# Performance work log

Measured on AMD Instinct MI355X. Metric: run time of the kernel, lower is better.

The kernel has to match this reference:

```python
import jax, jax.numpy as jnp
import numpy as np

NHEADS = 16
SCALE_BASE = 512
GN_EPS = 1e-5


def rotate_every_two(x):
    x1 = x[..., ::2]
    x2 = x[..., 1::2]
    return jnp.stack((-x2, x1), axis=-1).reshape(x.shape)


def xpos_apply(x, downscale, offset=0):
    # x: [B, T, C]; XPOS over the FULL embedding dim (applied before head split)
    B, T, C = x.shape
    half = C // 2
    scale_vec = (jnp.arange(0, C, 2, dtype=jnp.float32) + 0.4 * C) / (1.4 * C)  # [half]
    min_pos = -(T + offset) // 2
    max_pos = T + offset + min_pos
    power = jnp.arange(min_pos, max_pos, dtype=jnp.float32) / SCALE_BASE  # [L]
    scale = scale_vec[None, :] ** power[:, None]  # [L, half]
    L = scale.shape[0]
    inv_freq = 1.0 / (10000.0 ** (jnp.arange(half, dtype=jnp.float32) / half))
    sinusoid = jnp.arange(L, dtype=jnp.float32)[:, None] * inv_freq[None, :]  # [L, half]
    sin, cos = jnp.sin(sinusoid), jnp.cos(sinusoid)
    if L > T:
        scale, sin, cos = scale[-T:], sin[-T:], cos[-T:]
    if downscale:
        scale = 1.0 / scale
    sin = jnp.repeat(sin * scale, 2, axis=-1)  # [T, C] (duplicate_interleave)
    cos = jnp.repeat(cos * scale, 2, axis=-1)
    return x * cos + rotate_every_two(x) * sin


def decay_mask(nheads, T):
    gamma = 1.0 - 2.0 ** (-5.0 - jnp.arange(nheads, dtype=jnp.float32))  # [H]
    idx = jnp.arange(T)
    diff = idx[:, None] - idx[None, :]  # [T, T]
    keep = diff >= 0
    m = gamma[:, None, None] ** jnp.where(keep, diff, 0).astype(jnp.float32)
    return jnp.where(keep[None, :, :], m, 0.0)  # [H, T, T]


def setup_inputs() -> dict:
    key = jax.random.key(0)
    ks = jax.random.split(key, 6)
    B, T, C = 2, 2048, 1024
    w_std = 0.02
    return {
        "x": jax.random.normal(ks[0], (B, T, C), jnp.float32),
        "w_qkvff": jax.random.normal(ks[1], (5 * C, C), jnp.float32) * w_std,
        "w_gated": jax.random.normal(ks[2], (C, C), jnp.float32) * w_std,
        "b_gated": jnp.zeros((C,), jnp.float32),
        "w_proj": jax.random.normal(ks[3], (C, C), jnp.float32) * w_std,
        "b_proj": jnp.zeros((C,), jnp.float32),
        "gn_w": jnp.ones((C,), jnp.float32),
        "gn_b": jnp.zeros((C,), jnp.float32),
        "w_ff": jax.random.normal(ks[4], (C, 2 * C), jnp.float32) * w_std,
        "rms_w": jnp.ones((C,), jnp.float32),
    }


def reference(x, w_qkvff, w_gated, b_gated, w_proj, b_proj, gn_w, gn_b, w_ff, rms_w):
    B, T, C = x.shape
    H = NHEADS
    hd = C // H
    # RMSNorm: x / clamp(||x|| * C^-0.5, 1e-8) * w
    nrm = jnp.sqrt(jnp.sum(x * x, axis=-1, keepdims=True)) * (C ** -0.5)
    x_ = x / jnp.maximum(nrm, 1e-8) * rms_w
    # fused qkvff projection (Linear, no bias): [B,T,5C]
    qkvff = jnp.einsum('btc,oc->bto', x_, w_qkvff)
    q, k, v, ff = jnp.split(qkvff, [C, 2 * C, 3 * C], axis=-1)
    q = xpos_apply(q, downscale=False)
    k = xpos_apply(k, downscale=True)
    # split heads -> [B,H,T,hd]
    q = q.reshape(B, T, H, hd).transpose(0, 2, 1, 3)
    k = k.reshape(B, T, H, hd).transpose(0, 2, 1, 3)
    v = v.reshape(B, T, H, hd).transpose(0, 2, 1, 3)
    # parallel retention: decay-masked QK^T @ V
    scores = jnp.einsum('bhtd,bhsd->bhts', q, k) * (hd ** -0.5)
    scores = scores * decay_mask(H, T)[None]
    y = jnp.einsum('bhts,bhsd->bhtd', scores, v)  # [B,H,T,hd]
    # GroupNorm(H groups) applied over flattened (B*T, C)
    yg = y.transpose(0, 2, 1, 3).reshape(B * T, H, hd)
    mu = jnp.mean(yg, axis=-1, keepdims=True)
    var = jnp.mean((yg - mu) ** 2, axis=-1, keepdims=True)
    yg = (yg - mu) / jnp.sqrt(var + GN_EPS)
    y = yg.reshape(B * T, C) * gn_w + gn_b
    y = y.reshape(B, T, C)
    # gated SiLU on raw x (pre-norm), then output proj
    y = jax.nn.silu(jnp.einsum('btc,oc->bto', x, w_gated) + b_gated) * y
    y = jnp.einsum('btc,oc->bto', y, w_proj) + b_proj
    # gated FFN branch: exact (erf) GELU then Linear(2C->C, no bias)
    ff_out = jnp.einsum('bte,ce->btc', jax.nn.gelu(ff, approximate=False), w_ff)
    return x + ff_out + y
```

## Files before the change

### kernel.cpp

```cpp
#include <hip/hip_runtime.h>
#include <math.h>

#define B_  2
#define T_  2048
#define C_  1024
#define H_  16
#define FC_ 5120

typedef __attribute__((ext_vector_type(8))) short  s16x8;
typedef __attribute__((ext_vector_type(4))) float  f32x4;
typedef __attribute__((ext_vector_type(2))) unsigned short u16x2;
typedef __attribute__((ext_vector_type(4))) unsigned short u16x4;
typedef __attribute__((ext_vector_type(8))) unsigned short u16x8;

#define AS1 __attribute__((address_space(1)))
#define AS3 __attribute__((address_space(3)))

__device__ __forceinline__ ushort f2bf(float f) {
    union { float f; unsigned u; } v; v.f = f;
    unsigned r = v.u + 0x7FFFu + ((v.u >> 16) & 1u);
    return (ushort)(r >> 16);
}
__device__ __forceinline__ float bf2f(ushort u) {
    union { unsigned u; float f; } v; v.u = (unsigned)u << 16; return v.f;
}
__device__ __forceinline__ void gload16(const void* g, void* l) {
    __builtin_amdgcn_global_load_lds((const AS1 unsigned int*)g,
                                     (AS3 unsigned int*)l, 16, 0, 0);
}

__global__ __launch_bounds__(256) void cvt_all_kernel(
        const float* __restrict__ x, const float* __restrict__ wq,
        const float* __restrict__ wg, const float* __restrict__ wp,
        const float* __restrict__ wf,
        ushort* __restrict__ xb, ushort* __restrict__ wqb, ushort* __restrict__ wgb,
        ushort* __restrict__ wpb, ushort* __restrict__ wfb) {
    int i = blockIdx.x * 256 + threadIdx.x;
    const float* src; ushort* dst; int off;
    if (i < 524288)       { src = x;  dst = xb;  off = i; }
    else if (i < 1179648) { src = wq; dst = wqb; off = i - 524288; }
    else if (i < 1310720) { src = wg; dst = wgb; off = i - 1179648; }
    else if (i < 1441792) { src = wp; dst = wpb; off = i - 1310720; }
    else                  { src = wf; dst = wfb; off = i - 1441792; }
    float4 a = ((const float4*)src)[2*off];
    float4 b = ((const float4*)src)[2*off + 1];
    u16x8 o;
    o[0] = f2bf(a.x); o[1] = f2bf(a.y); o[2] = f2bf(a.z); o[3] = f2bf(a.w);
    o[4] = f2bf(b.x); o[5] = f2bf(b.y); o[6] = f2bf(b.z); o[7] = f2bf(b.w);
    *(u16x8*)(dst + 8*off) = o;
}

__global__ __launch_bounds__(256) void rmsnorm_kernel(const float* __restrict__ x,
                                                      const float* __restrict__ rms_w,
                                                      ushort* __restrict__ xn) {
    int row = blockIdx.x;
    int tid = threadIdx.x;
    float4 v = ((const float4*)(x + (size_t)row * C_))[tid];
    float ss = v.x*v.x + v.y*v.y + v.z*v.z + v.w*v.w;
    #pragma unroll
    for (int m = 32; m >= 1; m >>= 1) ss += __shfl_xor(ss, m);
    __shared__ float wsum[4];
    if ((tid & 63) == 0) wsum[tid >> 6] = ss;
    __syncthreads();
    float tot = wsum[0] + wsum[1] + wsum[2] + wsum[3];
    float nrm = sqrtf(tot) * 0.03125f;
    float inv = 1.0f / fmaxf(nrm, 1e-8f);
    float4 w = ((const float4*)rms_w)[tid];
    u16x4 o;
    o[0] = f2bf(v.x * inv * w.x);  o[1] = f2bf(v.y * inv * w.y);
    o[2] = f2bf(v.z * inv * w.z);  o[3] = f2bf(v.w * inv * w.w);
    *(u16x4*)(xn + (size_t)row * C_ + 4*tid) = o;
}

__global__ __launch_bounds__(256) void xpos_bf16_kernel(const ushort* __restrict__ qktmp,
                                                        ushort* __restrict__ qkv) {
    int bt = blockIdx.x;
    int t = bt & (T_ - 1);
    float tf = (float)t;
    const ushort* row = qktmp + (size_t)bt * 2048;
    ushort* orow = qkv + (size_t)bt * 3072;
    float power = (tf - 1024.0f) * (1.0f / 512.0f);
    for (int i = threadIdx.x; i < 512; i += 256) {
        float sv    = (2.0f * (float)i + 409.6f) * (1.0f / 1433.6f);
        float scale = exp2f(power * log2f(sv));
        float invf  = exp2f((float)i * (-13.287712379549449f / 512.0f));
        float ang   = tf * invf;
        float sn, cs;
        sincosf(ang, &sn, &cs);
        float rs = 1.0f / scale;
        int hh = i >> 5;
        float lg2g = log2f(1.0f - exp2f(-5.0f - (float)hh));
        float gq = exp2f(lg2g * tf) * 0.125f;
        float gk = exp2f(-lg2g * tf);
        u16x2 qi = *(const u16x2*)(row + 2*i);
        u16x2 ki = *(const u16x2*)(row + 1024 + 2*i);
        float qx = bf2f(qi[0]), qy = bf2f(qi[1]);
        float kx = bf2f(ki[0]), ky = bf2f(ki[1]);
        float qox = (qx*(cs*scale) - qy*(sn*scale)) * gq;
        float qoy = (qy*(cs*scale) + qx*(sn*scale)) * gq;
        float kox = (kx*(cs*rs) - ky*(sn*rs)) * gk;
        float koy = (ky*(cs*rs) + kx*(sn*rs)) * gk;
        u16x2 qo; qo[0] = f2bf(qox); qo[1] = f2bf(qoy);
        u16x2 ko; ko[0] = f2bf(kox); ko[1] = f2bf(koy);
        *(u16x2*)(orow + 2*i) = qo;
        *(u16x2*)(orow + 1024 + 2*i) = ko;
    }
}

template<int EPI, int BN>
__global__ __launch_bounds__(256) void gemm_bf16_kernel(
        const ushort* __restrict__ A, int lda,
        const ushort* __restrict__ W, int ldw,
        float* __restrict__ Cmat, int ldc, int K,
        const float* __restrict__ bias,
        const float* __restrict__ add1,
        const float* __restrict__ add2,
        ushort* __restrict__ oqk,
        ushort* __restrict__ ov,
        ushort* __restrict__ offb) {
    constexpr int NG = BN / 32;
    __shared__ __align__(16) ushort As[128*64];
    __shared__ __align__(16) ushort Bs[BN*64];
    int tid = threadIdx.x;
    int m0 = blockIdx.y * 128, n0 = blockIdx.x * BN;
    int wave = tid >> 6, lane = tid & 63;
    int lo = lane & 15, hi = lane >> 4;
    int wm = (wave >> 1) * 64, wn = (wave & 1) * (BN/2);
    int lrow  = lane >> 3;
    int gcol  = ((lane & 7) ^ lrow) * 8;
    f32x4 acc[4][NG] = {};

    for (int k0 = 0; k0 < K; k0 += 64) {
        __syncthreads();
        #pragma unroll
        for (int i = 0; i < 4; ++i) {
            int c = wave*4 + i;
            gload16(A + (size_t)(m0 + c*8 + lrow) * lda + k0 + gcol,
                    (ushort*)As + c*512);
        }
        if constexpr (BN == 128) {
            #pragma unroll
            for (int i = 0; i < 4; ++i) {
                int c = wave*4 + i;
                gload16(W + (size_t)(n0 + c*8 + lrow) * ldw + k0 + gcol,
                        (ushort*)Bs + c*512);
            }
        } else {
            #pragma unroll
            for (int i = 0; i < 2; ++i) {
                int c = wave*2 + i;
                gload16(W + (size_t)(n0 + c*8 + lrow) * ldw + k0 + gcol,
                        (ushort*)Bs + c*512);
            }
        }
        __syncthreads();
        #pragma unroll
        for (int kc = 0; kc < 2; ++kc) {
            s16x8 af[4], bf[NG];
            #pragma unroll
            for (int g = 0; g < 4; ++g) {
                int arow = wm + g*16 + lo;
                af[g] = *(const s16x8*)((const char*)As +
                         arow*128 + ((kc*64 + hi*16) ^ ((arow & 7) << 4)));
            }
            #pragma unroll
            for (int g = 0; g < NG; ++g) {
                int brow = wn + g*16 + lo;
                bf[g] = *(const s16x8*)((const char*)Bs +
                         brow*128 + ((kc*64 + hi*16) ^ ((brow & 7) << 4)));
            }
            #pragma unroll
            for (int mg = 0; mg < 4; ++mg)
                #pragma unroll
                for (int ng = 0; ng < NG; ++ng)
                    acc[mg][ng] = __builtin_amdgcn_mfma_f32_16x16x32_bf16(
                        af[mg], bf[ng], acc[mg][ng], 0, 0, 0);
        }
    }
    #pragma unroll
    for (int mg = 0; mg < 4; ++mg) {
        #pragma unroll
        for (int r = 0; r < 4; ++r) {
            size_t m = (size_t)(m0 + wm + mg*16 + hi*4 + r);
            #pragma unroll
            for (int ng = 0; ng < NG; ++ng) {
                int n = n0 + wn + ng*16 + lo;
                float v = acc[mg][ng][r];
                if constexpr (EPI == 3) {
                    if (n0 < 2048)      oqk[m*2048 + n] = f2bf(v);
                    else if (n0 < 3072) ov[m*3072 + n] = f2bf(v);
                    else offb[m*2048 + (n - 3072)] =
                             f2bf(0.5f * v * (1.0f + erff(v * 0.70710678118f)));
                } else {
                    if (EPI == 1) {
                        float s = v + bias[n];
                        v = s / (1.0f + expf(-s));
                    } else if (EPI == 2) {
                        v += bias[n] + add1[m*ldc + n] + add2[m*ldc + n];
                    }
                    Cmat[m*ldc + n] = v;
                }
            }
        }
    }
}

__global__ __launch_bounds__(256) void attn_mfma2_kernel(const ushort* __restrict__ qkv,
                                                         float* __restrict__ y) {
    __shared__ ushort Ks[2][64*64];
    __shared__ ushort Vt[2][64*64];
    __shared__ ushort Ss[4][16*64];
    int F = blockIdx.x;
    int o = (F & 7) * 64 + (F >> 3);
    int tta = o & 15;
    int h   = (o >> 4) & 15;
    int b   = o >> 8;
    int ttb = 31 - tta;
    int t0a = tta * 64, t0b = ttb * 64;
    int tid = threadIdx.x;
    int wave = tid >> 6, lane = tid & 63;
    int lo = lane & 15, hi = lane >> 4;
    const size_t bT = (size_t)b * T_;

    const ushort* qra = qkv + (bT + t0a + wave*16 + lo) * 3072 + h*64;
    const ushort* qrb = qkv + (bT + t0b + wave*16 + lo) * 3072 + h*64;
    s16x8 qa0 = *(const s16x8*)(qra + hi*8);
    s16x8 qa1 = *(const s16x8*)(qra + 32 + hi*8);
    s16x8 qb0 = *(const s16x8*)(qrb + hi*8);
    s16x8 qb1 = *(const s16x8*)(qrb + 32 + hi*8);
    f32x4 acca[4] = {}, accb[4] = {};

    int kr = tid >> 2, kc = tid & 3;
    int vd0 = (tid & 15) * 4, vs0 = (tid >> 4) * 4;
    u16x8 rka, rkb;
    u16x4 rv0, rv1, rv2, rv3;
    auto loadt = [&](int s0) {
        const ushort* src = qkv + (bT + s0 + kr) * 3072 + 1024 + h*64;
        rka = *(const u16x8*)(src + kc*8);
        rkb = *(const u16x8*)(src + (kc+4)*8);
        const ushort* vsrc = qkv + (bT + s0 + vs0) * 3072 + 2048 + h*64 + vd0;
        rv0 = *(const u16x4*)(vsrc);
        rv1 = *(const u16x4*)(vsrc + 3072);
        rv2 = *(const u16x4*)(vsrc + 2*3072);
        rv3 = *(const u16x4*)(vsrc + 3*3072);
    };
    int cur = 0;
    loadt(0);
    for (int st = 0; st <= ttb; ++st) {
        {
            int base = kr * 128, sw = (kr & 7) << 4;
            *(u16x8*)((char*)Ks[cur] + ((base + kc*16) ^ sw))     = rka;
            *(u16x8*)((char*)Ks[cur] + ((base + (kc+4)*16) ^ sw)) = rkb;
            #pragma unroll
            for (int i = 0; i < 4; ++i) {
                u16x4 o4; o4[0] = rv0[i]; o4[1] = rv1[i]; o4[2] = rv2[i]; o4[3] = rv3[i];
                int d = vd0 + i;
                *(u16x4*)((char*)Vt[cur] + ((d*128 + vs0*2) ^ ((d & 7) << 4))) = o4;
            }
        }
        __syncthreads();
        if (st < ttb) loadt((st + 1) * 64);

        auto compute = [&](s16x8 q0, s16x8 q1, f32x4* accy, bool diag) {
            f32x4 sacc[4] = {};
            #pragma unroll
            for (int sn = 0; sn < 4; ++sn) {
                int srow = sn*16 + lo;
                int rb2 = srow * 128, sw = (srow & 7) << 4;
                s16x8 kf0 = *(const s16x8*)((const char*)Ks[cur] + ((rb2 + hi*16) ^ sw));
                s16x8 kf1 = *(const s16x8*)((const char*)Ks[cur] + ((rb2 + 64 + hi*16) ^ sw));
                sacc[sn] = __builtin_amdgcn_mfma_f32_16x16x32_bf16(q0, kf0, sacc[sn], 0, 0, 0);
                sacc[sn] = __builtin_amdgcn_mfma_f32_16x16x32_bf16(q1, kf1, sacc[sn], 0, 0, 0);
            }
            #pragma unroll
            for (int sn = 0; sn < 4; ++sn) {
                int sl = sn*16 + lo;
                #pragma unroll
                for (int r = 0; r < 4; ++r) {
                    float v = sacc[sn][r];
                    if (diag && sl > wave*16 + hi*4 + r) v = 0.0f;
                    int tq = hi*4 + r;
                    *(ushort*)((char*)Ss[wave] + ((tq*128 + sl*2) ^ ((tq & 7) << 4))) = f2bf(v);
                }
            }
            s16x8 sa0 = *(const s16x8*)((const char*)Ss[wave] + ((lo*128 + hi*16) ^ ((lo & 7) << 4)));
            s16x8 sa1 = *(const s16x8*)((const char*)Ss[wave] + ((lo*128 + 64 + hi*16) ^ ((lo & 7) << 4)));
            #pragma unroll
            for (int dn = 0; dn < 4; ++dn) {
                int d = dn*16 + lo;
                int rb2 = d * 128, sw = (d & 7) << 4;
                s16x8 vf0 = *(const s16x8*)((const char*)Vt[cur] + ((rb2 + hi*16) ^ sw));
                s16x8 vf1 = *(const s16x8*)((const char*)Vt[cur] + ((rb2 + 64 + hi*16) ^ sw));
                accy[dn] = __builtin_amdgcn_mfma_f32_16x16x32_bf16(sa0, vf0, accy[dn], 0, 0, 0);
                accy[dn] = __builtin_amdgcn_mfma_f32_16x16x32_bf16(sa1, vf1, accy[dn], 0, 0, 0);
            }
        };
        compute(qb0, qb1, accb, st == ttb);
        if (st <= tta) compute(qa0, qa1, acca, st == tta);
        cur ^= 1;
    }
    #pragma unroll
    for (int dn = 0; dn < 4; ++dn) {
        #pragma unroll
        for (int r = 0; r < 4; ++r) {
            int ta = t0a + wave*16 + hi*4 + r;
            int tb = t0b + wave*16 + hi*4 + r;
            y[(bT + ta) * C_ + h*64 + dn*16 + lo] = acca[dn][r];
            y[(bT + tb) * C_ + h*64 + dn*16 + lo] = accb[dn][r];
        }
    }
}

__global__ __launch_bounds__(256) void gn_gate_kernel(const float* __restrict__ y,
                                                      const float* __restrict__ gate,
                                                      const float* __restrict__ gn_w,
                                                      const float* __restrict__ gn_b,
                                                      ushort* __restrict__ ygb) {
    int bt = blockIdx.x;
    int tid = threadIdx.x;
    float4 v = ((const float4*)(y + (size_t)bt * C_))[tid];
    float s1 = v.x + v.y + v.z + v.w;
    float s2 = v.x*v.x + v.y*v.y + v.z*v.z + v.w*v.w;
    #pragma unroll
    for (int m = 1; m < 16; m <<= 1) { s1 += __shfl_xor(s1, m); s2 += __shfl_xor(s2, m); }
    float mu   = s1 * (1.0f/64.0f);
    float var  = s2 * (1.0f/64.0f) - mu*mu;
    float rstd = rsqrtf(var + 1e-5f);
    float4 w  = ((const float4*)gn_w)[tid];
    float4 bb = ((const float4*)gn_b)[tid];
    float4 g  = ((const float4*)(gate + (size_t)bt * C_))[tid];
    u16x4 o;
    o[0] = f2bf(((v.x - mu)*rstd*w.x + bb.x) * g.x);
    o[1] = f2bf(((v.y - mu)*rstd*w.y + bb.y) * g.y);
    o[2] = f2bf(((v.z - mu)*rstd*w.z + bb.z) * g.z);
    o[3] = f2bf(((v.w - mu)*rstd*w.w + bb.w) * g.w);
    *(u16x4*)(ygb + (size_t)bt * C_ + 4*tid) = o;
}

extern "C" void kernel_launch(void* const* d_in, const int* in_sizes, int n_in,
                              void* d_out, int out_size, void* d_ws, size_t ws_size,
                              hipStream_t stream) {
    (void)in_sizes; (void)n_in; (void)out_size; (void)ws_size;
    const float* x       = (const float*)d_in[0];
    const float* w_qkvff = (const float*)d_in[1];
    const float* w_gated = (const float*)d_in[2];
    const float* b_gated = (const float*)d_in[3];
    const float* w_proj  = (const float*)d_in[4];
    const float* b_proj  = (const float*)d_in[5];
    const float* gn_w    = (const float*)d_in[6];
    const float* gn_b    = (const float*)d_in[7];
    const float* w_ff    = (const float*)d_in[8];
    const float* rms_w   = (const float*)d_in[9];
    float* out = (float*)d_out;

    const size_t NTOK = (size_t)B_ * T_;
    float* buf0   = (float*)d_ws;
    float* buf1   = buf0 + NTOK * C_;
    float* buf2   = buf1 + NTOK * C_;
    ushort* qkvb  = (ushort*)(buf2 + NTOK * C_);
    ushort* qktmp = qkvb + NTOK * 3072;
    ushort* xb    = qktmp + NTOK * 2048;
    ushort* xnb   = xb + NTOK * C_;
    ushort* ffb   = xnb + NTOK * C_;
    ushort* ygb   = ffb + NTOK * 2048;
    ushort* wqb   = ygb + NTOK * C_;
    ushort* wgb   = wqb + (size_t)FC_ * C_;
    ushort* wpb   = wgb + (size_t)C_ * C_;
    ushort* wfb   = wpb + (size_t)C_ * C_;

    cvt_all_kernel<<<6656, 256, 0, stream>>>(x, w_qkvff, w_gated, w_proj, w_ff,
                                             xb, wqb, wgb, wpb, wfb);
    rmsnorm_kernel<<<4096, 256, 0, stream>>>(x, rms_w, xnb);
    gemm_bf16_kernel<3,128><<<dim3(40, 32), 256, 0, stream>>>(
        xnb, C_, wqb, C_, nullptr, 0, C_, nullptr, nullptr, nullptr, qktmp, qkvb, ffb);
    xpos_bf16_kernel<<<4096, 256, 0, stream>>>(qktmp, qkvb);
    attn_mfma2_kernel<<<512, 256, 0, stream>>>(qkvb, buf1);
    gemm_bf16_kernel<1,64><<<dim3(16, 32), 256, 0, stream>>>(
        xb, C_, wgb, C_, buf2, C_, C_, b_gated, nullptr, nullptr, nullptr, nullptr, nullptr);
    gn_gate_kernel<<<4096, 256, 0, stream>>>(buf1, buf2, gn_w, gn_b, ygb);
    gemm_bf16_kernel<0,64><<<dim3(16, 32), 256, 0, stream>>>(
        ffb, 2*C_, wfb, 2*C_, buf0, C_, 2*C_, nullptr, nullptr, nullptr, nullptr, nullptr, nullptr);
    gemm_bf16_kernel<2,64><<<dim3(16, 32), 256, 0, stream>>>(
        ygb, C_, wpb, C_, out, C_, C_, b_proj, x, buf0, nullptr, nullptr, nullptr);
}
```

Before: 328.5 us.

## Fold RMSNorm into QKV GEMM epilogue, merge gate GEMM, double-buffer LDS

Folds the RMSNorm weight into the QKV/FF weight conversion and applies the per-row inverse norm in the GEMM epilogue, so one bf16 copy of x feeds both the QKV/FF projection and the gate projection. The gate GEMM is merged into the big projection as extra N columns (grid grows from 40 to 48 column tiles) and writes a bf16 SiLU gate, which drops one launch and an fp32 intermediate buffer. The GEMM also switches to double-buffered LDS with the next tile's load issued before the current tile's MFMAs, overlapping memory with compute. The costs are doubled LDS use, which can lower occupancy, and a bf16 gate that adds rounding error.

```diff
diff --git a/kernel.cpp b/kernel.cpp
--- a/kernel.cpp
+++ b/kernel.cpp
@@ -30,46 +30,51 @@
 }
 
 __global__ __launch_bounds__(256) void cvt_all_kernel(
-        const float* __restrict__ x, const float* __restrict__ wq,
-        const float* __restrict__ wg, const float* __restrict__ wp,
-        const float* __restrict__ wf,
-        ushort* __restrict__ xb, ushort* __restrict__ wqb, ushort* __restrict__ wgb,
+        const float* __restrict__ wq, const float* __restrict__ wg,
+        const float* __restrict__ wp, const float* __restrict__ wf,
+        const float* __restrict__ rms_w,
+        ushort* __restrict__ wqb, ushort* __restrict__ wgb,
         ushort* __restrict__ wpb, ushort* __restrict__ wfb) {
     int i = blockIdx.x * 256 + threadIdx.x;
-    const float* src; ushort* dst; int off;
-    if (i < 524288)       { src = x;  dst = xb;  off = i; }
-    else if (i < 1179648) { src = wq; dst = wqb; off = i - 524288; }
-    else if (i < 1310720) { src = wg; dst = wgb; off = i - 1179648; }
-    else if (i < 1441792) { src = wp; dst = wpb; off = i - 1310720; }
-    else                  { src = wf; dst = wfb; off = i - 1441792; }
+    const float* src; ushort* dst; int off; bool fold = false;
+    if (i < 655360)       { src = wq; dst = wqb; off = i; fold = true; }
+    else if (i < 786432)  { src = wg; dst = wgb; off = i - 655360; }
+    else if (i < 917504)  { src = wp; dst = wpb; off = i - 786432; }
+    else                  { src = wf; dst = wfb; off = i - 917504; }
     float4 a = ((const float4*)src)[2*off];
     float4 b = ((const float4*)src)[2*off + 1];
+    if (fold) {
+        int c = (off * 8) & 1023;
+        float4 r0 = *(const float4*)(rms_w + c);
+        float4 r1 = *(const float4*)(rms_w + c + 4);
+        a.x *= r0.x; a.y *= r0.y; a.z *= r0.z; a.w *= r0.w;
+        b.x *= r1.x; b.y *= r1.y; b.z *= r1.z; b.w *= r1.w;
+    }
     u16x8 o;
     o[0] = f2bf(a.x); o[1] = f2bf(a.y); o[2] = f2bf(a.z); o[3] = f2bf(a.w);
     o[4] = f2bf(b.x); o[5] = f2bf(b.y); o[6] = f2bf(b.z); o[7] = f2bf(b.w);
     *(u16x8*)(dst + 8*off) = o;
 }
 
-__global__ __launch_bounds__(256) void rmsnorm_kernel(const float* __restrict__ x,
-                                                      const float* __restrict__ rms_w,
-                                                      ushort* __restrict__ xn) {
+__global__ __launch_bounds__(256) void rmsx_kernel(const float* __restrict__ x,
+                                                   ushort* __restrict__ xb,
+                                                   float* __restrict__ inv_out) {
     int row = blockIdx.x;
     int tid = threadIdx.x;
     float4 v = ((const float4*)(x + (size_t)row * C_))[tid];
+    u16x4 o;
+    o[0] = f2bf(v.x); o[1] = f2bf(v.y); o[2] = f2bf(v.z); o[3] = f2bf(v.w);
+    *(u16x4*)(xb + (size_t)row * C_ + 4*tid) = o;
     float ss = v.x*v.x + v.y*v.y + v.z*v.z + v.w*v.w;
     #pragma unroll
     for (int m = 32; m >= 1; m >>= 1) ss += __shfl_xor(ss, m);
     __shared__ float wsum[4];
     if ((tid & 63) == 0) wsum[tid >> 6] = ss;
     __syncthreads();
-    float tot = wsum[0] + wsum[1] + wsum[2] + wsum[3];
-    float nrm = sqrtf(tot) * 0.03125f;
-    float inv = 1.0f / fmaxf(nrm, 1e-8f);
-    float4 w = ((const float4*)rms_w)[tid];
-    u16x4 o;
-    o[0] = f2bf(v.x * inv * w.x);  o[1] = f2bf(v.y * inv * w.y);
-    o[2] = f2bf(v.z * inv * w.z);  o[3] = f2bf(v.w * inv * w.w);
-    *(u16x4*)(xn + (size_t)row * C_ + 4*tid) = o;
+    if (tid == 0) {
+        float tot = wsum[0] + wsum[1] + wsum[2] + wsum[3];
+        inv_out[row] = 1.0f / fmaxf(sqrtf(tot) * 0.03125f, 1e-8f);
+    }
 }
 
 __global__ __launch_bounds__(256) void xpos_bf16_kernel(const ushort* __restrict__ qktmp,
@@ -115,12 +120,14 @@
         const float* __restrict__ bias,
         const float* __restrict__ add1,
         const float* __restrict__ add2,
+        const float* __restrict__ inv,
         ushort* __restrict__ oqk,
         ushort* __restrict__ ov,
-        ushort* __restrict__ offb) {
+        ushort* __restrict__ offb,
+        ushort* __restrict__ ogate) {
     constexpr int NG = BN / 32;
-    __shared__ __align__(16) ushort As[128*64];
-    __shared__ __align__(16) ushort Bs[BN*64];
+    __shared__ __align__(16) ushort As[2][128*64];
+    __shared__ __align__(16) ushort Bs[2][BN*64];
     int tid = threadIdx.x;
     int m0 = blockIdx.y * 128, n0 = blockIdx.x * BN;
     int wave = tid >> 6, lane = tid & 63;
@@ -130,43 +137,49 @@
     int gcol  = ((lane & 7) ^ lrow) * 8;
     f32x4 acc[4][NG] = {};
 
-    for (int k0 = 0; k0 < K; k0 += 64) {
-        __syncthreads();
+    auto stage = [&](int k0, int buf) {
         #pragma unroll
         for (int i = 0; i < 4; ++i) {
             int c = wave*4 + i;
             gload16(A + (size_t)(m0 + c*8 + lrow) * lda + k0 + gcol,
-                    (ushort*)As + c*512);
+                    (ushort*)As[buf] + c*512);
         }
         if constexpr (BN == 128) {
             #pragma unroll
             for (int i = 0; i < 4; ++i) {
                 int c = wave*4 + i;
                 gload16(W + (size_t)(n0 + c*8 + lrow) * ldw + k0 + gcol,
-                        (ushort*)Bs + c*512);
+                        (ushort*)Bs[buf] + c*512);
             }
         } else {
             #pragma unroll
             for (int i = 0; i < 2; ++i) {
                 int c = wave*2 + i;
                 gload16(W + (size_t)(n0 + c*8 + lrow) * ldw + k0 + gcol,
-                        (ushort*)Bs + c*512);
-            }
-        }
-        __syncthreads();
+                        (ushort*)Bs[buf] + c*512);
+            }
+        }
+    };
+
+    int cur = 0;
+    stage(0, 0);
+    __syncthreads();
+    for (int k0 = 0;;) {
+        int nxt = k0 + 64;
+        if (nxt < K) stage(nxt, cur ^ 1);
         #pragma unroll
         for (int kc = 0; kc < 2; ++kc) {
             s16x8 af[4], bf[NG];
             #pragma unroll
             for (int g = 0; g < 4; ++g) {
                 int arow = wm + g*16 + lo;
-                af[g] = *(const s16x8*)((const char*)As +
+                af[g] = *(const s16x8*)((const char*)As[cur] +
                          arow*128 + ((kc*64 + hi*16) ^ ((arow & 7) << 4)));
             }
             #pragma unroll
             for (int g = 0; g < NG; ++g) {
                 int brow = wn + g*16 + lo;
-                bf[g] = *(const s16x8*)((const char*)Bs +
+                bf[g] = *(const s16x8*)((const char*)Bs[cur] +
                          brow*128 + ((kc*64 + hi*16) ^ ((brow & 7) << 4)));
             }
             #pragma unroll
@@ -176,28 +189,35 @@
                     acc[mg][ng] = __builtin_amdgcn_mfma_f32_16x16x32_bf16(
                         af[mg], bf[ng], acc[mg][ng], 0, 0, 0);
         }
+        if (nxt >= K) break;
+        __syncthreads();
+        cur ^= 1; k0 = nxt;
     }
     #pragma unroll
     for (int mg = 0; mg < 4; ++mg) {
         #pragma unroll
         for (int r = 0; r < 4; ++r) {
             size_t m = (size_t)(m0 + wm + mg*16 + hi*4 + r);
+            float iv = 1.0f;
+            if constexpr (EPI == 4) iv = inv[m];
             #pragma unroll
             for (int ng = 0; ng < NG; ++ng) {
                 int n = n0 + wn + ng*16 + lo;
                 float v = acc[mg][ng][r];
-                if constexpr (EPI == 3) {
-                    if (n0 < 2048)      oqk[m*2048 + n] = f2bf(v);
-                    else if (n0 < 3072) ov[m*3072 + n] = f2bf(v);
-                    else offb[m*2048 + (n - 3072)] =
-                             f2bf(0.5f * v * (1.0f + erff(v * 0.70710678118f)));
+                if constexpr (EPI == 4) {
+                    if (n0 < 2048)      oqk[m*2048 + n] = f2bf(v * iv);
+                    else if (n0 < 3072) ov[m*3072 + n] = f2bf(v * iv);
+                    else if (n0 < 5120) {
+                        float g = v * iv;
+                        offb[m*2048 + (n - 3072)] =
+                            f2bf(0.5f * g * (1.0f + erff(g * 0.70710678118f)));
+                    } else {
+                        float s = v + bias[n - 5120];
+                        ogate[m*1024 + (n - 5120)] = f2bf(s / (1.0f + expf(-s)));
+                    }
                 } else {
-                    if (EPI == 1) {
-                        float s = v + bias[n];
-                        v = s / (1.0f + expf(-s));
-                    } else if (EPI == 2) {
+                    if (EPI == 2)
                         v += bias[n] + add1[m*ldc + n] + add2[m*ldc + n];
-                    }
                     Cmat[m*ldc + n] = v;
                 }
             }
@@ -312,7 +332,7 @@
 }
 
 __global__ __launch_bounds__(256) void gn_gate_kernel(const float* __restrict__ y,
-                                                      const float* __restrict__ gate,
+                                                      const ushort* __restrict__ gateb,
                                                       const float* __restrict__ gn_w,
                                                       const float* __restrict__ gn_b,
                                                       ushort* __restrict__ ygb) {
@@ -328,12 +348,12 @@
     float rstd = rsqrtf(var + 1e-5f);
     float4 w  = ((const float4*)gn_w)[tid];
     float4 bb = ((const float4*)gn_b)[tid];
-    float4 g  = ((const float4*)(gate + (size_t)bt * C_))[tid];
+    u16x4 g4 = *(const u16x4*)(gateb + (size_t)bt * C_ + 4*tid);
     u16x4 o;
-    o[0] = f2bf(((v.x - mu)*rstd*w.x + bb.x) * g.x);
-    o[1] = f2bf(((v.y - mu)*rstd*w.y + bb.y) * g.y);
-    o[2] = f2bf(((v.z - mu)*rstd*w.z + bb.z) * g.z);
-    o[3] = f2bf(((v.w - mu)*rstd*w.w + bb.w) * g.w);
+    o[0] = f2bf(((v.x - mu)*rstd*w.x + bb.x) * bf2f(g4[0]));
+    o[1] = f2bf(((v.y - mu)*rstd*w.y + bb.y) * bf2f(g4[1]));
+    o[2] = f2bf(((v.z - mu)*rstd*w.z + bb.z) * bf2f(g4[2]));
+    o[3] = f2bf(((v.w - mu)*rstd*w.w + bb.w) * bf2f(g4[3]));
     *(u16x4*)(ygb + (size_t)bt * C_ + 4*tid) = o;
 }
 
@@ -356,30 +376,31 @@
     const size_t NTOK = (size_t)B_ * T_;
     float* buf0   = (float*)d_ws;
     float* buf1   = buf0 + NTOK * C_;
-    float* buf2   = buf1 + NTOK * C_;
-    ushort* qkvb  = (ushort*)(buf2 + NTOK * C_);
+    ushort* qkvb  = (ushort*)(buf1 + NTOK * C_);
     ushort* qktmp = qkvb + NTOK * 3072;
     ushort* xb    = qktmp + NTOK * 2048;
-    ushort* xnb   = xb + NTOK * C_;
-    ushort* ffb   = xnb + NTOK * C_;
+    ushort* ffb   = xb + NTOK * C_;
     ushort* ygb   = ffb + NTOK * 2048;
-    ushort* wqb   = ygb + NTOK * C_;
+    ushort* gateb = ygb + NTOK * C_;
+    ushort* wqb   = gateb + NTOK * C_;
     ushort* wgb   = wqb + (size_t)FC_ * C_;
     ushort* wpb   = wgb + (size_t)C_ * C_;
     ushort* wfb   = wpb + (size_t)C_ * C_;
-
-    cvt_all_kernel<<<6656, 256, 0, stream>>>(x, w_qkvff, w_gated, w_proj, w_ff,
-                                             xb, wqb, wgb, wpb, wfb);
-    rmsnorm_kernel<<<4096, 256, 0, stream>>>(x, rms_w, xnb);
-    gemm_bf16_kernel<3,128><<<dim3(40, 32), 256, 0, stream>>>(
-        xnb, C_, wqb, C_, nullptr, 0, C_, nullptr, nullptr, nullptr, qktmp, qkvb, ffb);
+    float* inv    = (float*)(wfb + (size_t)C_ * 2*C_);
+
+    cvt_all_kernel<<<4608, 256, 0, stream>>>(w_qkvff, w_gated, w_proj, w_ff, rms_w,
+                                             wqb, wgb, wpb, wfb);
+    rmsx_kernel<<<4096, 256, 0, stream>>>(x, xb, inv);
+    gemm_bf16_kernel<4,128><<<dim3(48, 32), 256, 0, stream>>>(
+        xb, C_, wqb, C_, nullptr, 0, C_, b_gated, nullptr, nullptr, inv,
+        qktmp, qkvb, ffb, gateb);
     xpos_bf16_kernel<<<4096, 256, 0, stream>>>(qktmp, qkvb);
     attn_mfma2_kernel<<<512, 256, 0, stream>>>(qkvb, buf1);
-    gemm_bf16_kernel<1,64><<<dim3(16, 32), 256, 0, stream>>>(
-        xb, C_, wgb, C_, buf2, C_, C_, b_gated, nullptr, nullptr, nullptr, nullptr, nullptr);
-    gn_gate_kernel<<<4096, 256, 0, stream>>>(buf1, buf2, gn_w, gn_b, ygb);
+    gn_gate_kernel<<<4096, 256, 0, stream>>>(buf1, gateb, gn_w, gn_b, ygb);
     gemm_bf16_kernel<0,64><<<dim3(16, 32), 256, 0, stream>>>(
-        ffb, 2*C_, wfb, 2*C_, buf0, C_, 2*C_, nullptr, nullptr, nullptr, nullptr, nullptr, nullptr);
+        ffb, 2*C_, wfb, 2*C_, buf0, C_, 2*C_, nullptr, nullptr, nullptr, nullptr,
+        nullptr, nullptr, nullptr, nullptr);
     gemm_bf16_kernel<2,64><<<dim3(16, 32), 256, 0, stream>>>(
-        ygb, C_, wpb, C_, out, C_, C_, b_proj, x, buf0, nullptr, nullptr, nullptr);
-}
+        ygb, C_, wpb, C_, out, C_, C_, b_proj, x, buf0, nullptr,
+        nullptr, nullptr, nullptr, nullptr);
+}
```

Result: slower. 350.2 us (+6.6%).
